# Kernel tuning notes

Hardware: AMD Instinct MI355X
Metric: run time of the kernel (lower is better)

Reference implementation:

```python
import jax, jax.numpy as jnp
import numpy as np

NUM_CODES = 16
BOOK_SIZE = 1024
EMBED_DIM = 64
BATCH = 8192


def setup_inputs() -> dict:
    key = jax.random.key(0)
    k1, k2 = jax.random.split(key)
    x = jax.random.normal(k1, (BATCH, NUM_CODES * EMBED_DIM), dtype=jnp.float32)
    codebook = jax.random.normal(k2, (NUM_CODES, BOOK_SIZE, EMBED_DIM), dtype=jnp.float32)
    return {"x": x, "codebook": codebook}


def reference(x, codebook):
    # VQVAE.quantise: per-code squared cdist to codebook, argmin, gather, one-hot.
    B = x.shape[0]
    nc, bs, d = codebook.shape
    xr = x.reshape(B, nc, d)                                   # [B, nc, d]
    x2 = jnp.sum(xr * xr, axis=-1)                             # [B, nc]
    c2 = jnp.sum(codebook * codebook, axis=-1)                 # [nc, bs]
    xc = jnp.einsum('bnd,nkd->bnk', xr, codebook)              # [B, nc, bs]
    dist = x2[:, :, None] - 2.0 * xc + c2[None, :, :]          # [B, nc, bs]
    idx = jnp.argmin(dist, axis=-1)                            # [B, nc]
    # gather quantised codes: codebook[n, idx[b, n]] -> [B, nc, d]
    cw = codebook[jnp.arange(nc)[None, :], idx]
    cw_embed = cw.reshape(B, nc * d)
    one_hot_idx = jax.nn.one_hot(idx, bs, dtype=x.dtype)       # [B, nc, bs]
    return cw_embed, one_hot_idx
```

## Files before the change

kernel.cpp:

```cpp
#include <hip/hip_runtime.h>
#include <hip/hip_bf16.h>

constexpr int NC    = 16;
constexpr int BS    = 1024;
constexpr int D     = 64;
constexpr int BATCH = 8192;
constexpr int BM    = 64;
constexpr int BK    = 128;
constexpr int NCH   = BS / BK;

constexpr int XT_P = 68;
constexpr int CT_P = 132;

constexpr size_t EMBED_ELEMS = (size_t)BATCH * NC * D;

typedef float vf4 __attribute__((ext_vector_type(4)));

__device__ __forceinline__ float mulrn(float a, float b) {
  float r = a * b; asm volatile("" : "+v"(r)); return r;
}
__device__ __forceinline__ float addrn(float a, float b) {
  float r = a + b; asm volatile("" : "+v"(r)); return r;
}
__device__ __forceinline__ float subrn(float a, float b) {
  float r = a - b; asm volatile("" : "+v"(r)); return r;
}


__device__ __forceinline__ float np_einsum_dot(const float* x0, const float* c) {
  float S0 = mulrn(x0[0 * XT_P], c[0]);
  float S1 = mulrn(x0[1 * XT_P], c[1]);
  float S2 = mulrn(x0[2 * XT_P], c[2]);
  float S3 = mulrn(x0[3 * XT_P], c[3]);
  #pragma unroll
  for (int t = 1; t < 16; ++t) {
    S0 = addrn(S0, mulrn(x0[(4 * t + 0) * XT_P], c[4 * t + 0]));
    S1 = addrn(S1, mulrn(x0[(4 * t + 1) * XT_P], c[4 * t + 1]));
    S2 = addrn(S2, mulrn(x0[(4 * t + 2) * XT_P], c[4 * t + 2]));
    S3 = addrn(S3, mulrn(x0[(4 * t + 3) * XT_P], c[4 * t + 3]));
  }
  return addrn(addrn(S0, S1), addrn(S2, S3));
}

template <int STRIDE>
__device__ __forceinline__ float np_sumsq(const float* p) {
  float s[4];
  #pragma unroll
  for (int j = 0; j < 4; ++j) {
    float r[8];
    #pragma unroll
    for (int v = 0; v < 8; ++v) {
      const float a0 = p[(4 * v + j) * STRIDE];
      const float a1 = p[(32 + 4 * v + j) * STRIDE];
      r[v] = addrn(mulrn(a0, a0), mulrn(a1, a1));
    }
    s[j] = addrn(addrn(addrn(r[0], r[1]), addrn(r[2], r[3])),
                 addrn(addrn(r[4], r[5]), addrn(r[6], r[7])));
  }
  return addrn(addrn(s[0], s[1]), addrn(s[2], s[3]));
}

__device__ __forceinline__ float np_dist(const float* x0, const float* c, float x2n) {
  const float xc  = np_einsum_dot(x0, c);
  const float c2n = np_sumsq<1>(c);
  return addrn(subrn(x2n, mulrn(2.0f, xc)), c2n);
}

__global__ __launch_bounds__(256, 2) void vq_kernel(
    const float* __restrict__ x,
    const float* __restrict__ cb,
    float* __restrict__ out)
{
  __shared__ float Xs[D][XT_P];
  __shared__ float Cs[D][CT_P];
  __shared__ float c2s[BK];
  __shared__ int   idxs[BM];

  const int tid = threadIdx.x;
  const int tx  = tid & 15;
  const int ty  = tid >> 4;
  const int n   = blockIdx.y;
  const int rb  = blockIdx.x * BM;

  const float* __restrict__ cbn = cb + (size_t)n * BS * D;

  {
    const float* xb = x + (size_t)rb * (NC * D) + (size_t)n * D;
    const int r = tid >> 2;
    const int b = tid & 3;
    #pragma unroll
    for (int i = 0; i < 4; ++i) {
      const int d4 = b * 4 + i * 16;
      float4 v = *reinterpret_cast<const float4*>(xb + (size_t)r * (NC * D) + d4);
      Xs[d4 + 0][r] = v.x;
      Xs[d4 + 1][r] = v.y;
      Xs[d4 + 2][r] = v.z;
      Xs[d4 + 3][r] = v.w;
    }
  }

  float v1[4], v2[4];
  int   k1[4], k2[4];
  #pragma unroll
  for (int i = 0; i < 4; ++i) { v1[i] = 3.0e38f; v2[i] = 3.0e38f; k1[i] = 0; k2[i] = 0; }

  for (int ch = 0; ch < NCH; ++ch) {
    __syncthreads();
    {
      const float* cbase = cbn + (size_t)(ch * BK) * D;
      const int c0 = tid >> 2;
      const int b  = tid & 3;
      #pragma unroll
      for (int i = 0; i < 8; ++i) {
        const int cc = c0 + (i & 1) * 64;
        const int d4 = b * 4 + (i >> 1) * 16;
        float4 v = *reinterpret_cast<const float4*>(cbase + (size_t)cc * D + d4);
        Cs[d4 + 0][cc] = v.x;
        Cs[d4 + 1][cc] = v.y;
        Cs[d4 + 2][cc] = v.z;
        Cs[d4 + 3][cc] = v.w;
      }
    }
    __syncthreads();
    if (tid < BK) {
      float s = 0.f;
      #pragma unroll
      for (int kk = 0; kk < D; ++kk) { float c = Cs[kk][tid]; s = fmaf(c, c, s); }
      c2s[tid] = s;
    }
    __syncthreads();

    float acc[4][8];
    #pragma unroll
    for (int i = 0; i < 4; ++i)
      #pragma unroll
      for (int j = 0; j < 8; ++j) acc[i][j] = 0.f;

    #pragma unroll 8
    for (int kk = 0; kk < D; ++kk) {
      float4 xa = *reinterpret_cast<const float4*>(&Xs[kk][ty * 4]);
      float4 c0 = *reinterpret_cast<const float4*>(&Cs[kk][tx * 4]);
      float4 c1 = *reinterpret_cast<const float4*>(&Cs[kk][64 + tx * 4]);
      const float xs[4]  = {xa.x, xa.y, xa.z, xa.w};
      const float csv[8] = {c0.x, c0.y, c0.z, c0.w, c1.x, c1.y, c1.z, c1.w};
      #pragma unroll
      for (int i = 0; i < 4; ++i)
        #pragma unroll
        for (int j = 0; j < 8; ++j)
          acc[i][j] = fmaf(xs[i], csv[j], acc[i][j]);
    }

    #pragma unroll
    for (int i = 0; i < 4; ++i) {
      #pragma unroll
      for (int j = 0; j < 8; ++j) {
        const int col = (j < 4) ? (tx * 4 + j) : (64 + tx * 4 + (j - 4));
        const float s = fmaf(-2.f, acc[i][j], c2s[col]);
        const int k = ch * BK + col;
        const bool lt1 = (s < v1[i]);
        const bool lt2 = (s < v2[i]);
        v2[i] = lt1 ? v1[i] : (lt2 ? s : v2[i]);
        k2[i] = lt1 ? k1[i] : (lt2 ? k : k2[i]);
        v1[i] = lt1 ? s : v1[i];
        k1[i] = lt1 ? k : k1[i];
      }
    }
  }

  #pragma unroll 1
  for (int i = 0; i < 4; ++i) {
    float a1 = v1[i], a2 = v2[i];
    int   b1 = k1[i], b2 = k2[i];
    #pragma unroll
    for (int m = 1; m <= 8; m <<= 1) {
      const float o1 = __shfl_xor(a1, m);
      const int   p1 = __shfl_xor(b1, m);
      const float o2 = __shfl_xor(a2, m);
      const int   p2 = __shfl_xor(b2, m);
      if (o1 < a1 || (o1 == a1 && p1 < b1)) {
        float n2; int q2;
        if (a1 < o2 || (a1 == o2 && b1 < p2)) { n2 = a1; q2 = b1; }
        else                                  { n2 = o2; q2 = p2; }
        a1 = o1; b1 = p1; a2 = n2; b2 = q2;
      } else {
        if (o1 < a2 || (o1 == a2 && p1 < b2)) { a2 = o1; b2 = p1; }
      }
    }
    int winner = b1;
    if (!(a2 - a1 > 0.05f)) {
      const int r = ty * 4 + i;
      const float* x0 = &Xs[0][r];
      const float x2n = np_sumsq<XT_P>(x0);

      float bestv = np_dist(x0, cbn + (size_t)k1[i] * D, x2n);
      int   bestk = k1[i];
      const float d2 = np_dist(x0, cbn + (size_t)k2[i] * D, x2n);
      if (d2 < bestv || (d2 == bestv && k2[i] < bestk)) { bestv = d2; bestk = k2[i]; }

      #pragma unroll
      for (int m = 1; m <= 8; m <<= 1) {
        const float ov = __shfl_xor(bestv, m);
        const int   ok = __shfl_xor(bestk, m);
        if (ov < bestv || (ov == bestv && ok < bestk)) { bestv = ov; bestk = ok; }
      }
      winner = bestk;
    }
    if (tx == 0) idxs[ty * 4 + i] = winner;
  }
  __syncthreads();

  {
    const int r = tid >> 2;
    const int q = tid & 3;
    const int k = idxs[r];
    const float* src = cbn + (size_t)k * D + q * 16;
    float* dst = out + (size_t)(rb + r) * (NC * D) + (size_t)n * D + q * 16;
    #pragma unroll
    for (int j = 0; j < 4; ++j) {
      float4 v = *reinterpret_cast<const float4*>(src + 4 * j);
      vf4 w = {v.x, v.y, v.z, v.w};
      __builtin_nontemporal_store(w, reinterpret_cast<vf4*>(dst + 4 * j));
    }
  }

  {
    float* oh = out + EMBED_ELEMS;
    const int base = tid * 4;
    for (int r = 0; r < BM; ++r) {
      const int k = idxs[r];
      vf4 v;
      v.x = (k == base + 0) ? 1.f : 0.f;
      v.y = (k == base + 1) ? 1.f : 0.f;
      v.z = (k == base + 2) ? 1.f : 0.f;
      v.w = (k == base + 3) ? 1.f : 0.f;
      float* dst = oh + (size_t)(rb + r) * (NC * BS) + (size_t)n * BS + base;
      __builtin_nontemporal_store(v, reinterpret_cast<vf4*>(dst));
    }
  }
}

extern "C" void kernel_launch(void* const* d_in, const int* in_sizes, int n_in,
                              void* d_out, int out_size, void* d_ws, size_t ws_size,
                              hipStream_t stream) {
  const float* x  = (const float*)d_in[0];
  const float* cb = (const float*)d_in[1];
  float* out = (float*)d_out;
  dim3 grid(BATCH / BM, NC);
  vq_kernel<<<grid, dim3(256), 0, stream>>>(x, cb, out);
}
```

Baseline: 776.4 us.

## Compute distances with split-bf16 MFMA and a precomputed codebook split

Replaces the FP32 FMA outer-product distance computation with bf16x3 (hi/lo split) MFMA 16x16x32 instructions. A new pre-kernel splits the codebook into bf16 hi/lo halves and precomputes codeword norms in workspace, so the main kernel loads half-width data and skips per-chunk norm computation. X is split in-kernel. The FP32 refinement threshold is widened to absorb the extra error, and the exact-recheck now reads x from global memory; this adds a second launch and some risk of argmin mismatches.

```diff
diff --git a/kernel.cpp b/kernel.cpp
--- a/kernel.cpp
+++ b/kernel.cpp
@@ -6,15 +6,18 @@
 constexpr int D     = 64;
 constexpr int BATCH = 8192;
 constexpr int BM    = 64;
-constexpr int BK    = 128;
-constexpr int NCH   = BS / BK;
-
-constexpr int XT_P = 68;
-constexpr int CT_P = 132;
+constexpr int CC    = 128;
+constexpr int NCH   = BS / CC;
+constexpr int PS    = 88;
 
 constexpr size_t EMBED_ELEMS = (size_t)BATCH * NC * D;
+constexpr size_t CB_ELEMS    = (size_t)NC * BS * D;
 
 typedef float vf4 __attribute__((ext_vector_type(4)));
+typedef float floatx4 __attribute__((ext_vector_type(4)));
+typedef short short8 __attribute__((ext_vector_type(8)));
+typedef unsigned short u16;
+typedef u16 u16x8 __attribute__((ext_vector_type(8)));
 
 __device__ __forceinline__ float mulrn(float a, float b) {
   float r = a * b; asm volatile("" : "+v"(r)); return r;
@@ -26,23 +29,21 @@
   float r = a - b; asm volatile("" : "+v"(r)); return r;
 }
 
-
 __device__ __forceinline__ float np_einsum_dot(const float* x0, const float* c) {
-  float S0 = mulrn(x0[0 * XT_P], c[0]);
-  float S1 = mulrn(x0[1 * XT_P], c[1]);
-  float S2 = mulrn(x0[2 * XT_P], c[2]);
-  float S3 = mulrn(x0[3 * XT_P], c[3]);
+  float S0 = mulrn(x0[0], c[0]);
+  float S1 = mulrn(x0[1], c[1]);
+  float S2 = mulrn(x0[2], c[2]);
+  float S3 = mulrn(x0[3], c[3]);
   #pragma unroll
   for (int t = 1; t < 16; ++t) {
-    S0 = addrn(S0, mulrn(x0[(4 * t + 0) * XT_P], c[4 * t + 0]));
-    S1 = addrn(S1, mulrn(x0[(4 * t + 1) * XT_P], c[4 * t + 1]));
-    S2 = addrn(S2, mulrn(x0[(4 * t + 2) * XT_P], c[4 * t + 2]));
-    S3 = addrn(S3, mulrn(x0[(4 * t + 3) * XT_P], c[4 * t + 3]));
+    S0 = addrn(S0, mulrn(x0[4 * t + 0], c[4 * t + 0]));
+    S1 = addrn(S1, mulrn(x0[4 * t + 1], c[4 * t + 1]));
+    S2 = addrn(S2, mulrn(x0[4 * t + 2], c[4 * t + 2]));
+    S3 = addrn(S3, mulrn(x0[4 * t + 3], c[4 * t + 3]));
   }
   return addrn(addrn(S0, S1), addrn(S2, S3));
 }
 
-template <int STRIDE>
 __device__ __forceinline__ float np_sumsq(const float* p) {
   float s[4];
   #pragma unroll
@@ -50,8 +51,8 @@
     float r[8];
     #pragma unroll
     for (int v = 0; v < 8; ++v) {
-      const float a0 = p[(4 * v + j) * STRIDE];
-      const float a1 = p[(32 + 4 * v + j) * STRIDE];
+      const float a0 = p[4 * v + j];
+      const float a1 = p[32 + 4 * v + j];
       r[v] = addrn(mulrn(a0, a0), mulrn(a1, a1));
     }
     s[j] = addrn(addrn(addrn(r[0], r[1]), addrn(r[2], r[3])),
@@ -62,42 +63,113 @@
 
 __device__ __forceinline__ float np_dist(const float* x0, const float* c, float x2n) {
   const float xc  = np_einsum_dot(x0, c);
-  const float c2n = np_sumsq<1>(c);
+  const float c2n = np_sumsq(c);
   return addrn(subrn(x2n, mulrn(2.0f, xc)), c2n);
+}
+
+__device__ __forceinline__ u16 f2bf(float f) {
+  unsigned u = __float_as_uint(f);
+  return (u16)((u + 0x7FFFu + ((u >> 16) & 1u)) >> 16);
+}
+__device__ __forceinline__ float bf2f(u16 h) {
+  return __uint_as_float(((unsigned)h) << 16);
+}
+
+__global__ __launch_bounds__(256) void split_kernel(
+    const float* __restrict__ cb, u16* __restrict__ wh, u16* __restrict__ wl,
+    float* __restrict__ wc2)
+{
+  const int t    = blockIdx.x * 256 + threadIdx.x;
+  const int cand = t >> 2;
+  const int part = t & 3;
+  const float* src = cb + (size_t)cand * D + part * 16;
+  u16 hh[16], ll[16];
+  float ss = 0.f;
+  #pragma unroll
+  for (int i = 0; i < 4; ++i) {
+    float4 v = *reinterpret_cast<const float4*>(src + 4 * i);
+    const float fv[4] = {v.x, v.y, v.z, v.w};
+    #pragma unroll
+    for (int j = 0; j < 4; ++j) {
+      const float f = fv[j];
+      const u16 h = f2bf(f);
+      const float lo = f - bf2f(h);
+      hh[4 * i + j] = h;
+      ll[4 * i + j] = f2bf(lo);
+      ss = fmaf(f, f, ss);
+    }
+  }
+  u16* dh = wh + (size_t)cand * D + part * 16;
+  u16* dl = wl + (size_t)cand * D + part * 16;
+  *reinterpret_cast<u16x8*>(dh)     = *reinterpret_cast<u16x8*>(&hh[0]);
+  *reinterpret_cast<u16x8*>(dh + 8) = *reinterpret_cast<u16x8*>(&hh[8]);
+  *reinterpret_cast<u16x8*>(dl)     = *reinterpret_cast<u16x8*>(&ll[0]);
+  *reinterpret_cast<u16x8*>(dl + 8) = *reinterpret_cast<u16x8*>(&ll[8]);
+  ss += __shfl_xor(ss, 1);
+  ss += __shfl_xor(ss, 2);
+  if (part == 0) wc2[cand] = ss;
 }
 
 __global__ __launch_bounds__(256, 2) void vq_kernel(
     const float* __restrict__ x,
     const float* __restrict__ cb,
+    const u16* __restrict__ wh, const u16* __restrict__ wl,
+    const float* __restrict__ wc2,
     float* __restrict__ out)
 {
-  __shared__ float Xs[D][XT_P];
-  __shared__ float Cs[D][CT_P];
-  __shared__ float c2s[BK];
+  __shared__ u16   XhS[BM * PS];
+  __shared__ u16   XlS[BM * PS];
+  __shared__ u16   ChS[CC * PS];
+  __shared__ u16   ClS[CC * PS];
+  __shared__ float c2s[BS];
   __shared__ int   idxs[BM];
 
-  const int tid = threadIdx.x;
-  const int tx  = tid & 15;
-  const int ty  = tid >> 4;
-  const int n   = blockIdx.y;
-  const int rb  = blockIdx.x * BM;
+  const int tid  = threadIdx.x;
+  const int wave = tid >> 6;
+  const int lane = tid & 63;
+  const int g    = lane >> 4;
+  const int tx   = lane & 15;
+  const int n    = blockIdx.y;
+  const int rb   = blockIdx.x * BM;
 
   const float* __restrict__ cbn = cb + (size_t)n * BS * D;
+  const u16*   __restrict__ whn = wh + (size_t)n * BS * D;
+  const u16*   __restrict__ wln = wl + (size_t)n * BS * D;
+
+  *reinterpret_cast<float4*>(&c2s[tid * 4]) =
+      *reinterpret_cast<const float4*>(wc2 + (size_t)n * BS + tid * 4);
 
   {
-    const float* xb = x + (size_t)rb * (NC * D) + (size_t)n * D;
     const int r = tid >> 2;
     const int b = tid & 3;
+    const float* xr = x + (size_t)(rb + r) * (NC * D) + (size_t)n * D + b * 16;
+    u16 hh[16], ll[16];
     #pragma unroll
     for (int i = 0; i < 4; ++i) {
-      const int d4 = b * 4 + i * 16;
-      float4 v = *reinterpret_cast<const float4*>(xb + (size_t)r * (NC * D) + d4);
-      Xs[d4 + 0][r] = v.x;
-      Xs[d4 + 1][r] = v.y;
-      Xs[d4 + 2][r] = v.z;
-      Xs[d4 + 3][r] = v.w;
-    }
-  }
+      float4 v = *reinterpret_cast<const float4*>(xr + 4 * i);
+      const float fv[4] = {v.x, v.y, v.z, v.w};
+      #pragma unroll
+      for (int j = 0; j < 4; ++j) {
+        const float f = fv[j];
+        const u16 h = f2bf(f);
+        hh[4 * i + j] = h;
+        ll[4 * i + j] = f2bf(f - bf2f(h));
+      }
+    }
+    u16* dh = &XhS[r * PS + b * 16];
+    u16* dl = &XlS[r * PS + b * 16];
+    *reinterpret_cast<u16x8*>(dh)     = *reinterpret_cast<u16x8*>(&hh[0]);
+    *reinterpret_cast<u16x8*>(dh + 8) = *reinterpret_cast<u16x8*>(&hh[8]);
+    *reinterpret_cast<u16x8*>(dl)     = *reinterpret_cast<u16x8*>(&ll[0]);
+    *reinterpret_cast<u16x8*>(dl + 8) = *reinterpret_cast<u16x8*>(&ll[8]);
+  }
+  __syncthreads();
+
+  const int wr = wave * 16;
+  short8 ah0 = *reinterpret_cast<const short8*>(&XhS[(wr + tx) * PS + g * 8]);
+  short8 ah1 = *reinterpret_cast<const short8*>(&XhS[(wr + tx) * PS + g * 8 + 32]);
+  short8 al0 = *reinterpret_cast<const short8*>(&XlS[(wr + tx) * PS + g * 8]);
+  short8 al1 = *reinterpret_cast<const short8*>(&XlS[(wr + tx) * PS + g * 8 + 32]);
 
   float v1[4], v2[4];
   int   k1[4], k2[4];
@@ -107,70 +179,56 @@
   for (int ch = 0; ch < NCH; ++ch) {
     __syncthreads();
     {
-      const float* cbase = cbn + (size_t)(ch * BK) * D;
-      const int c0 = tid >> 2;
-      const int b  = tid & 3;
+      const int cl = tid >> 1;
+      const int hf = tid & 1;
+      const size_t gofs = (size_t)(ch * CC + cl) * D + hf * 32;
+      const u16* sh = whn + gofs;
+      const u16* sl = wln + gofs;
+      u16* dh = &ChS[cl * PS + hf * 32];
+      u16* dl = &ClS[cl * PS + hf * 32];
       #pragma unroll
-      for (int i = 0; i < 8; ++i) {
-        const int cc = c0 + (i & 1) * 64;
-        const int d4 = b * 4 + (i >> 1) * 16;
-        float4 v = *reinterpret_cast<const float4*>(cbase + (size_t)cc * D + d4);
-        Cs[d4 + 0][cc] = v.x;
-        Cs[d4 + 1][cc] = v.y;
-        Cs[d4 + 2][cc] = v.z;
-        Cs[d4 + 3][cc] = v.w;
+      for (int j = 0; j < 4; ++j) {
+        *reinterpret_cast<u16x8*>(dh + 8 * j) = *reinterpret_cast<const u16x8*>(sh + 8 * j);
+        *reinterpret_cast<u16x8*>(dl + 8 * j) = *reinterpret_cast<const u16x8*>(sl + 8 * j);
       }
     }
     __syncthreads();
-    if (tid < BK) {
-      float s = 0.f;
+
+    #pragma unroll
+    for (int t = 0; t < 8; ++t) {
+      const int cbase = t * 16;
+      const short8 bh0 = *reinterpret_cast<const short8*>(&ChS[(cbase + tx) * PS + g * 8]);
+      const short8 bh1 = *reinterpret_cast<const short8*>(&ChS[(cbase + tx) * PS + g * 8 + 32]);
+      const short8 bl0 = *reinterpret_cast<const short8*>(&ClS[(cbase + tx) * PS + g * 8]);
+      const short8 bl1 = *reinterpret_cast<const short8*>(&ClS[(cbase + tx) * PS + g * 8 + 32]);
+
+      floatx4 acc = {0.f, 0.f, 0.f, 0.f};
+      acc = __builtin_amdgcn_mfma_f32_16x16x32_bf16(ah0, bh0, acc, 0, 0, 0);
+      acc = __builtin_amdgcn_mfma_f32_16x16x32_bf16(ah1, bh1, acc, 0, 0, 0);
+      acc = __builtin_amdgcn_mfma_f32_16x16x32_bf16(ah0, bl0, acc, 0, 0, 0);
+      acc = __builtin_amdgcn_mfma_f32_16x16x32_bf16(ah1, bl1, acc, 0, 0, 0);
+      acc = __builtin_amdgcn_mfma_f32_16x16x32_bf16(al0, bh0, acc, 0, 0, 0);
+      acc = __builtin_amdgcn_mfma_f32_16x16x32_bf16(al1, bh1, acc, 0, 0, 0);
+
+      const int  k   = ch * CC + cbase + tx;
+      const float c2v = c2s[k];
       #pragma unroll
-      for (int kk = 0; kk < D; ++kk) { float c = Cs[kk][tid]; s = fmaf(c, c, s); }
-      c2s[tid] = s;
-    }
-    __syncthreads();
-
-    float acc[4][8];
-    #pragma unroll
-    for (int i = 0; i < 4; ++i)
-      #pragma unroll
-      for (int j = 0; j < 8; ++j) acc[i][j] = 0.f;
-
-    #pragma unroll 8
-    for (int kk = 0; kk < D; ++kk) {
-      float4 xa = *reinterpret_cast<const float4*>(&Xs[kk][ty * 4]);
-      float4 c0 = *reinterpret_cast<const float4*>(&Cs[kk][tx * 4]);
-      float4 c1 = *reinterpret_cast<const float4*>(&Cs[kk][64 + tx * 4]);
-      const float xs[4]  = {xa.x, xa.y, xa.z, xa.w};
-      const float csv[8] = {c0.x, c0.y, c0.z, c0.w, c1.x, c1.y, c1.z, c1.w};
-      #pragma unroll
-      for (int i = 0; i < 4; ++i)
-        #pragma unroll
-        for (int j = 0; j < 8; ++j)
-          acc[i][j] = fmaf(xs[i], csv[j], acc[i][j]);
-    }
-
-    #pragma unroll
-    for (int i = 0; i < 4; ++i) {
-      #pragma unroll
-      for (int j = 0; j < 8; ++j) {
-        const int col = (j < 4) ? (tx * 4 + j) : (64 + tx * 4 + (j - 4));
-        const float s = fmaf(-2.f, acc[i][j], c2s[col]);
-        const int k = ch * BK + col;
-        const bool lt1 = (s < v1[i]);
-        const bool lt2 = (s < v2[i]);
-        v2[i] = lt1 ? v1[i] : (lt2 ? s : v2[i]);
-        k2[i] = lt1 ? k1[i] : (lt2 ? k : k2[i]);
-        v1[i] = lt1 ? s : v1[i];
-        k1[i] = lt1 ? k : k1[i];
+      for (int reg = 0; reg < 4; ++reg) {
+        const float s = fmaf(-2.f, acc[reg], c2v);
+        const bool lt1 = (s < v1[reg]);
+        const bool lt2 = (s < v2[reg]);
+        v2[reg] = lt1 ? v1[reg] : (lt2 ? s : v2[reg]);
+        k2[reg] = lt1 ? k1[reg] : (lt2 ? k : k2[reg]);
+        v1[reg] = lt1 ? s : v1[reg];
+        k1[reg] = lt1 ? k : k1[reg];
       }
     }
   }
 
   #pragma unroll 1
-  for (int i = 0; i < 4; ++i) {
-    float a1 = v1[i], a2 = v2[i];
-    int   b1 = k1[i], b2 = k2[i];
+  for (int reg = 0; reg < 4; ++reg) {
+    float a1 = v1[reg], a2 = v2[reg];
+    int   b1 = k1[reg], b2 = k2[reg];
     #pragma unroll
     for (int m = 1; m <= 8; m <<= 1) {
       const float o1 = __shfl_xor(a1, m);
@@ -186,17 +244,15 @@
         if (o1 < a2 || (o1 == a2 && p1 < b2)) { a2 = o1; b2 = p1; }
       }
     }
+    const int row_local = wr + g * 4 + reg;
     int winner = b1;
-    if (!(a2 - a1 > 0.05f)) {
-      const int r = ty * 4 + i;
-      const float* x0 = &Xs[0][r];
-      const float x2n = np_sumsq<XT_P>(x0);
-
-      float bestv = np_dist(x0, cbn + (size_t)k1[i] * D, x2n);
-      int   bestk = k1[i];
-      const float d2 = np_dist(x0, cbn + (size_t)k2[i] * D, x2n);
-      if (d2 < bestv || (d2 == bestv && k2[i] < bestk)) { bestv = d2; bestk = k2[i]; }
-
+    if (!(a2 - a1 > 0.08f)) {
+      const float* xrow = x + (size_t)(rb + row_local) * (NC * D) + (size_t)n * D;
+      const float x2n = np_sumsq(xrow);
+      float bestv = np_dist(xrow, cbn + (size_t)k1[reg] * D, x2n);
+      int   bestk = k1[reg];
+      const float dd = np_dist(xrow, cbn + (size_t)k2[reg] * D, x2n);
+      if (dd < bestv || (dd == bestv && k2[reg] < bestk)) { bestv = dd; bestk = k2[reg]; }
       #pragma unroll
       for (int m = 1; m <= 8; m <<= 1) {
         const float ov = __shfl_xor(bestv, m);
@@ -205,7 +261,7 @@
       }
       winner = bestk;
     }
-    if (tx == 0) idxs[ty * 4 + i] = winner;
+    if (tx == 0) idxs[row_local] = winner;
   }
   __syncthreads();
 
@@ -245,6 +301,12 @@
   const float* x  = (const float*)d_in[0];
   const float* cb = (const float*)d_in[1];
   float* out = (float*)d_out;
+
+  u16*   wh  = (u16*)d_ws;
+  u16*   wl  = wh + CB_ELEMS;
+  float* wc2 = (float*)(wl + CB_ELEMS);
+
+  split_kernel<<<dim3(256), dim3(256), 0, stream>>>(cb, wh, wl, wc2);
   dim3 grid(BATCH / BM, NC);
-  vq_kernel<<<grid, dim3(256), 0, stream>>>(x, cb, out);
-}
+  vq_kernel<<<grid, dim3(256), 0, stream>>>(x, cb, wh, wl, wc2, out);
+}
```

Result: faster. 711.6 us (-8.3%).
